# Kernel optimization log

Hardware: AMD Instinct MI355X
Metric: run time of the kernel (lower is better)

## Reference

```python
import jax, jax.numpy as jnp
import numpy as np

NS = 50000; ND = 50000; E = 600000
C = 64; A = 16; S = 64; H = 8; M = 192; DH = C // H
EPS = 1e-5


def _ln(x, w, b):
    # EquivariantLayerNormV2 restricted to 0e irreps == standard affine LayerNorm
    x = x - jnp.mean(x, axis=-1, keepdims=True)
    v = jnp.mean(x * x, axis=-1, keepdims=True)
    return x * jax.lax.rsqrt(v + EPS) * w + b


def _forward(src_f, dst_f, edge_attr, edge_scalars, edge_logits, edge_src, edge_dst,
             ln_src_w, ln_src_b, W_src, ln_dst_w, ln_dst_b, W_dst, b_dst,
             W_ea, W_dtp, W_r1, b_r1, W_r2, b_r2, alpha_vec,
             W_proj, b_proj, ln_post_w, ln_post_b, W_f1, b_f1, W_f2, b_f2):
    # prenorm + linear projections of src/dst node features
    ms = _ln(src_f, ln_src_w, ln_src_b) @ W_src                      # [NS, C]
    md = _ln(dst_f, ln_dst_w, ln_dst_b) @ W_dst + b_dst              # [ND, C]
    msg = ms[edge_src] + md[edge_dst]                                # [E, C] gather
    # radial MLP on edge scalars modulates the (scalar-irrep) tensor-product weights
    r = jax.nn.silu(edge_scalars @ W_r1 + b_r1)                      # [E, S]
    w_edge = r @ W_r2 + b_r2                                         # [E, 2C]
    ea = edge_attr @ W_ea                                            # [E, C]
    dtp = ((msg * ea) @ W_dtp) * w_edge                              # [E, 2C]
    alpha_feat = dtp[:, :C].reshape(E, H, DH)
    val = dtp[:, C:].reshape(E, H, DH)
    # per-head attention logits + optional precomputed edge logits
    logits = jnp.sum(jax.nn.leaky_relu(alpha_feat, 0.2) * alpha_vec, axis=-1)  # [E, H]
    logits = logits + edge_logits[:, None]
    # softmax over incoming edges of each dst node (segment softmax)
    m = jax.ops.segment_max(logits, edge_dst, num_segments=ND)
    a = jnp.exp(logits - m[edge_dst])
    z = jax.ops.segment_sum(a, edge_dst, num_segments=ND)
    attn = a / z[edge_dst]                                           # [E, H]
    out = jax.ops.segment_sum((val * attn[..., None]).reshape(E, C), edge_dst,
                              num_segments=ND)                       # [ND, C] scatter
    out = out @ W_proj + b_proj
    emb = out + dst_f                                                # skip_1 (irreps match -> identity)
    y = _ln(emb, ln_post_w, ln_post_b)                               # post_norm
    ffn = jax.nn.silu(y @ W_f1 + b_f1) @ W_f2 + b_f2                 # FFN with swish gate (0e)
    return ffn + emb                                                 # skip_2


def setup_inputs() -> dict:
    key = jax.random.key(0)
    ks = jax.random.split(key, 20)
    def n(k, shape, scale=1.0):
        return jax.random.normal(k, shape, dtype=jnp.float32) * scale
    return {
        "src_f": n(ks[0], (NS, C)),
        "dst_f": n(ks[1], (ND, C)),
        "edge_attr": n(ks[2], (E, A)),
        "edge_scalars": jax.random.uniform(ks[3], (E, S), dtype=jnp.float32),
        "edge_logits": n(ks[4], (E,)),
        "edge_src": jax.random.randint(ks[5], (E,), 0, NS),
        "edge_dst": jax.random.randint(ks[6], (E,), 0, ND),
        "ln_src_w": jnp.ones((C,), jnp.float32), "ln_src_b": jnp.zeros((C,), jnp.float32),
        "W_src": n(ks[7], (C, C), C ** -0.5),
        "ln_dst_w": jnp.ones((C,), jnp.float32), "ln_dst_b": jnp.zeros((C,), jnp.float32),
        "W_dst": n(ks[8], (C, C), C ** -0.5), "b_dst": jnp.zeros((C,), jnp.float32),
        "W_ea": n(ks[9], (A, C), A ** -0.5),
        "W_dtp": n(ks[10], (C, 2 * C), C ** -0.5),
        "W_r1": n(ks[11], (S, S), S ** -0.5), "b_r1": jnp.zeros((S,), jnp.float32),
        "W_r2": n(ks[12], (S, 2 * C), S ** -0.5), "b_r2": jnp.zeros((2 * C,), jnp.float32),
        "alpha_vec": n(ks[13], (H, DH), DH ** -0.5),
        "W_proj": n(ks[14], (C, C), C ** -0.5), "b_proj": jnp.zeros((C,), jnp.float32),
        "ln_post_w": jnp.ones((C,), jnp.float32), "ln_post_b": jnp.zeros((C,), jnp.float32),
        "W_f1": n(ks[15], (C, M), C ** -0.5), "b_f1": jnp.zeros((M,), jnp.float32),
        "W_f2": n(ks[16], (M, C), M ** -0.5), "b_f2": jnp.zeros((C,), jnp.float32),
    }


def reference(src_f, dst_f, edge_attr, edge_scalars, edge_logits, edge_src, edge_dst,
              ln_src_w, ln_src_b, W_src, ln_dst_w, ln_dst_b, W_dst, b_dst,
              W_ea, W_dtp, W_r1, b_r1, W_r2, b_r2, alpha_vec,
              W_proj, b_proj, ln_post_w, ln_post_b, W_f1, b_f1, W_f2, b_f2):
    return _forward(src_f, dst_f, edge_attr, edge_scalars, edge_logits, edge_src, edge_dst,
                    ln_src_w, ln_src_b, W_src, ln_dst_w, ln_dst_b, W_dst, b_dst,
                    W_ea, W_dtp, W_r1, b_r1, W_r2, b_r2, alpha_vec,
                    W_proj, b_proj, ln_post_w, ln_post_b, W_f1, b_f1, W_f2, b_f2)
```

## Files before the change

kernel.cpp:

```cpp
#include <hip/hip_runtime.h>
#include <hip/hip_bf16.h>

typedef __hip_bfloat16 bf16;
typedef unsigned short u16;
typedef unsigned int u32;

#define NS_N 50000
#define ND_N 50000
#define NE_E 600000
#define C 64
#define AD 16
#define SD 64
#define NH 8
#define MF 192
#define EPSV 1e-5f

#define WB() __builtin_amdgcn_wave_barrier()

typedef short short8 __attribute__((ext_vector_type(8)));
typedef float f32x4 __attribute__((ext_vector_type(4)));
#define MFMA16(a, b, c) __builtin_amdgcn_mfma_f32_16x16x32_bf16(a, b, c, 0, 0, 0)

__device__ __forceinline__ float lo16(u32 u) {
    union { u32 i; float f; } v; v.i = u << 16; return v.f;
}
__device__ __forceinline__ float hi16(u32 u) {
    union { u32 i; float f; } v; v.i = u & 0xffff0000u; return v.f;
}
__device__ __forceinline__ float b2fu(u16 u) {
    union { u32 i; float f; } v; v.i = ((u32)u) << 16; return v.f;
}
__device__ __forceinline__ u16 f2bbits(float f) {
    u32 u = __float_as_uint(f);
    u32 r = u + 0x7FFFu + ((u >> 16) & 1u);
    return (u16)(r >> 16);
}
__device__ __forceinline__ float loadf(const void* p, size_t i, int isbf) {
    if (isbf) { union { u32 u; float f; } v; v.u = ((u32)((const u16*)p)[i]) << 16; return v.f; }
    return ((const float*)p)[i];
}
__device__ __forceinline__ u16 loadb(const void* p, size_t i, int isbf) {
    if (isbf) return ((const u16*)p)[i];
    return f2bbits(((const float*)p)[i]);
}
__device__ __forceinline__ short8 load8bf(const void* p, size_t off, int isbf) {
    if (isbf) return *(const short8*)((const u16*)p + off);
    const float4* q = (const float4*)((const float*)p + off);
    float4 f0 = q[0], f1 = q[1];
    short8 r;
    r[0] = (short)f2bbits(f0.x); r[1] = (short)f2bbits(f0.y);
    r[2] = (short)f2bbits(f0.z); r[3] = (short)f2bbits(f0.w);
    r[4] = (short)f2bbits(f1.x); r[5] = (short)f2bbits(f1.y);
    r[6] = (short)f2bbits(f1.z); r[7] = (short)f2bbits(f1.w);
    return r;
}

__device__ __forceinline__ float waveAllSum(float v) {
    #pragma unroll
    for (int off = 32; off >= 1; off >>= 1) v += __shfl_xor(v, off, 64);
    return v;
}

__global__ void detect_zero_kernel(const void* src, int* flag, int* cnt) {
    if (blockIdx.x == 0) {
        if (threadIdx.x < 64) {
            const u16* p = (const u16*)src;
            const int lane = threadIdx.x;
            int c = 0;
            #pragma unroll
            for (int j = 0; j < 32; ++j) {
                u16 w = p[(size_t)(lane * 32 + j) * 2];
                int e = (w >> 7) & 0xFF;
                if (w == 0 || (e >= 100 && e <= 150)) c++;
            }
            #pragma unroll
            for (int off = 32; off >= 1; off >>= 1) c += __shfl_xor(c, off, 64);
            if (lane == 0) *flag = (c > 1536) ? 1 : 0;
        }
    } else {
        int i = (blockIdx.x - 1) * blockDim.x + threadIdx.x;
        if (i < ND_N) cnt[i] = 0;
    }
}

__global__ void hist_kernel(const int* __restrict__ edge_dst, int* __restrict__ cnt) {
    int e = blockIdx.x * blockDim.x + threadIdx.x;
    if (e < NE_E) atomicAdd(&cnt[edge_dst[e]], 1);
}

#define SCAN_CHUNK 1024
#define SCAN_NCH ((ND_N + SCAN_CHUNK - 1) / SCAN_CHUNK)

__global__ void scan_phase1(const int* __restrict__ cnt, int* __restrict__ chunksum) {
    __shared__ int wsum[4];
    const int b = blockIdx.x, tidx = threadIdx.x;
    const int base = b * SCAN_CHUNK + tidx * 4;
    int s = 0;
    if (base + 3 < ND_N) {
        int4 v = *(const int4*)&cnt[base];
        s = v.x + v.y + v.z + v.w;
    } else {
        #pragma unroll
        for (int j = 0; j < 4; ++j) { int i = base + j; if (i < ND_N) s += cnt[i]; }
    }
    #pragma unroll
    for (int off = 32; off >= 1; off >>= 1) s += __shfl_xor(s, off, 64);
    const int wv = tidx >> 6, lane = tidx & 63;
    if (lane == 0) wsum[wv] = s;
    __syncthreads();
    if (tidx == 0) chunksum[b] = wsum[0] + wsum[1] + wsum[2] + wsum[3];
}

__global__ void scan_phase3(const int* __restrict__ cnt, const int* __restrict__ chunksum,
                            int* __restrict__ row_ptr, int* __restrict__ cursor,
                            int* __restrict__ row_ptr_last) {
    __shared__ int woff[4];
    __shared__ int choff_s;
    const int b = blockIdx.x, tidx = threadIdx.x;
    if (tidx < 64) {
        int v = (tidx < SCAN_NCH) ? chunksum[tidx] : 0;
        int incl = v;
        #pragma unroll
        for (int off = 1; off < 64; off <<= 1) {
            int t = __shfl_up(incl, off, 64);
            if (tidx >= off) incl += t;
        }
        if (tidx == b) choff_s = incl - v;
        if (b == 0 && tidx == 63) *row_ptr_last = incl;
    }
    const int base = b * SCAN_CHUNK + tidx * 4;
    int v[4];
    #pragma unroll
    for (int j = 0; j < 4; ++j) { int i = base + j; v[j] = (i < ND_N) ? cnt[i] : 0; }
    int s = v[0] + v[1] + v[2] + v[3];
    int incl = s;
    const int lane = tidx & 63, wv = tidx >> 6;
    #pragma unroll
    for (int off = 1; off < 64; off <<= 1) {
        int t = __shfl_up(incl, off, 64);
        if (lane >= off) incl += t;
    }
    if (lane == 63) woff[wv] = incl;
    __syncthreads();
    int cross = 0;
    for (int w = 0; w < wv; ++w) cross += woff[w];
    int run = choff_s + cross + (incl - s);
    #pragma unroll
    for (int j = 0; j < 4; ++j) {
        int i = base + j;
        if (i < ND_N) { row_ptr[i] = run; cursor[i] = run; }
        run += v[j];
    }
}

__global__ void scatter_kernel(const int* __restrict__ edge_dst, int* __restrict__ cursor,
                               int* __restrict__ perm) {
    int e = blockIdx.x * blockDim.x + threadIdx.x;
    if (e < NE_E) {
        int pos = atomicAdd(&cursor[edge_dst[e]], 1);
        perm[pos] = e;
    }
}

__global__ void node_proj2_kernel(const void* __restrict__ src_f, const void* __restrict__ dst_f,
                                  const void* __restrict__ lnw_s, const void* __restrict__ lnb_s,
                                  const void* __restrict__ W_s,
                                  const void* __restrict__ lnw_d, const void* __restrict__ lnb_d,
                                  const void* __restrict__ W_d, const void* __restrict__ b_d,
                                  const int* __restrict__ flagp,
                                  u16* __restrict__ ms, u16* __restrict__ md) {
    __shared__ u16 sW[C * C];
    __shared__ float slnw[C], slnb[C], sbias[C];
    __shared__ float ybuf[4][C];

    const int isbf = *flagp;
    const int tid = threadIdx.x;
    const int half = gridDim.x >> 1;
    const int isrc = (blockIdx.x < half) ? 1 : 0;
    const void* xf  = isrc ? src_f : dst_f;
    const void* lnw = isrc ? lnw_s : lnw_d;
    const void* lnb = isrc ? lnb_s : lnb_d;
    const void* W   = isrc ? W_s : W_d;
    u16* out        = isrc ? ms : md;
    const int N     = isrc ? NS_N : ND_N;
    const int bid   = isrc ? blockIdx.x : blockIdx.x - half;
    const int nb    = isrc ? half : gridDim.x - half;

    for (int i = tid; i < C * C; i += blockDim.x) {
        int k = i >> 6, c = i & 63;
        sW[((k >> 1) << 7) + (c << 1) + (k & 1)] = loadb(W, i, isbf);
    }
    if (tid < C) {
        slnw[tid] = loadf(lnw, tid, isbf);
        slnb[tid] = loadf(lnb, tid, isbf);
        sbias[tid] = isrc ? 0.f : loadf(b_d, tid, isbf);
    }
    __syncthreads();

    const int wave = tid >> 6, lane = tid & 63;
    const u32* w = (const u32*)sW;
    const int gw = bid * 4 + wave, nw = nb * 4;
    for (int n = gw; n < N; n += nw) {
        float x = loadf(xf, (size_t)n * C + lane, isbf);
        float mean = waveAllSum(x) * (1.f / 64.f);
        float xc = x - mean;
        float var = waveAllSum(xc * xc) * (1.f / 64.f);
        float y = xc * rsqrtf(var + EPSV) * slnw[lane] + slnb[lane];
        WB();
        ybuf[wave][lane] = y;
        WB();
        float acc = sbias[lane];
        #pragma unroll 8
        for (int k2 = 0; k2 < 32; ++k2) {
            float2 yv = *(const float2*)&ybuf[wave][k2 * 2];
            u32 wp = w[(k2 << 6) + lane];
            acc += yv.x * lo16(wp) + yv.y * hi16(wp);
        }
        WB();
        out[(size_t)n * C + lane] = f2bbits(acc);
        WB();
    }
}

__launch_bounds__(512, 4)
__global__ void edge_mfma_kernel(const void* __restrict__ edge_attr,
                                 const void* __restrict__ edge_scalars,
                                 const void* __restrict__ edge_logits,
                                 const int* __restrict__ edge_src,
                                 const int* __restrict__ edge_dst,
                                 const int* __restrict__ perm,
                                 const void* __restrict__ W_ea, const void* __restrict__ W_dtp,
                                 const void* __restrict__ W_r1, const void* __restrict__ b_r1,
                                 const void* __restrict__ W_r2, const void* __restrict__ b_r2,
                                 const void* __restrict__ alpha_vec,
                                 const int* __restrict__ flagp,
                                 const u16* __restrict__ ms, const u16* __restrict__ md,
                                 u16* __restrict__ valbuf, float* __restrict__ logitsbuf) {
    __shared__ u16 sWr1T[C * SD];
    __shared__ u16 sWr2T[2 * C * SD];
    __shared__ u16 sWdtpT[2 * C * C];
    __shared__ u16 sWeaT[C * 32];
    __shared__ float sbr1[SD], sbr2[2 * C], salpha[C];
    __shared__ u16 scratch[8][2][16 * C];

    const int isbf = *flagp;
    const int tid = threadIdx.x;
    for (int i = tid; i < SD * SD; i += 512) {
        int k = i >> 6, n = i & 63;
        sWr1T[n * 64 + (((k >> 3) ^ (n & 7)) << 3) + (k & 7)] = loadb(W_r1, i, isbf);
    }
    for (int i = tid; i < SD * 2 * C; i += 512) {
        int k = i >> 7, n = i & 127;
        sWr2T[n * 64 + (((k >> 3) ^ (n & 7)) << 3) + (k & 7)] = loadb(W_r2, i, isbf);
    }
    for (int i = tid; i < C * 2 * C; i += 512) {
        int k = i >> 7, n = i & 127;
        sWdtpT[n * 64 + (((k >> 3) ^ (n & 7)) << 3) + (k & 7)] = loadb(W_dtp, i, isbf);
    }
    for (int i = tid; i < C * 32; i += 512) {
        int n = i >> 5, k = i & 31;
        sWeaT[i] = (k < AD) ? loadb(W_ea, (size_t)k * C + n, isbf) : (u16)0;
    }
    for (int i = tid; i < SD; i += 512) sbr1[i] = loadf(b_r1, i, isbf);
    for (int i = tid; i < 2 * C; i += 512) sbr2[i] = loadf(b_r2, i, isbf);
    for (int i = tid; i < C; i += 512) salpha[i] = loadf(alpha_vec, i, isbf);
    __syncthreads();

    const int wv = tid >> 6, lane = tid & 63;
    const int m15 = lane & 15, quad = lane >> 4;
    const int sw = m15 & 7;
    const int pg0 = (quad ^ sw) << 3;
    const int pg1 = pg0 ^ 32;
    u16* scr_r = scratch[wv][0];
    u16* scr_e = scratch[wv][1];

    const int NT = NE_E / 16;
    const int stride = gridDim.x * 8;
    int t = blockIdx.x * 8 + wv;

    int e = 0, s = 0, dd = 0;
    if (t < NT) {
        e = perm[t * 16 + m15];
        s = edge_src[e];
        dd = edge_dst[e];
    }

    while (t < NT) {
        const int tn = t + stride;
        const int e0 = t * 16;
        short8 esA0 = load8bf(edge_scalars, (size_t)e * SD + quad * 8, isbf);
        short8 esA1 = load8bf(edge_scalars, (size_t)e * SD + 32 + quad * 8, isbf);
        float elg_lane = loadf(edge_logits, e, isbf);
        short8 eaA = 0;
        if (quad < 2) eaA = load8bf(edge_attr, (size_t)e * AD + quad * 8, isbf);
        const u16* msr = ms + (size_t)s * C;
        const u16* mdr = md + (size_t)dd * C;
        short8 gms0 = *(const short8*)&msr[quad * 8];
        short8 gms1 = *(const short8*)&msr[32 + quad * 8];
        short8 gmd0 = *(const short8*)&mdr[quad * 8];
        short8 gmd1 = *(const short8*)&mdr[32 + quad * 8];
        int eN = 0;
        if (tn < NT) eN = perm[tn * 16 + m15];
        WB();
        #pragma unroll
        for (int nt = 0; nt < 4; ++nt) {
            f32x4 c = {0.f, 0.f, 0.f, 0.f};
            c = MFMA16(esA0, *(const short8*)&sWr1T[(nt * 16 + m15) * 64 + pg0], c);
            c = MFMA16(esA1, *(const short8*)&sWr1T[(nt * 16 + m15) * 64 + pg1], c);
            float bc = sbr1[nt * 16 + m15];
            int lg = nt * 2 + (m15 >> 3);
            int o = m15 & 7;
            #pragma unroll
            for (int r = 0; r < 4; ++r) {
                float f = c[r] + bc;
                f = f / (1.f + __expf(-f));
                int row = quad * 4 + r;
                scr_r[row * 64 + ((lg ^ (row & 7)) << 3) + o] = f2bbits(f);
            }
        }
        #pragma unroll
        for (int nt = 0; nt < 4; ++nt) {
            f32x4 c = {0.f, 0.f, 0.f, 0.f};
            c = MFMA16(eaA, *(const short8*)&sWeaT[(nt * 16 + m15) * 32 + quad * 8], c);
            int lg = nt * 2 + (m15 >> 3);
            int o = m15 & 7;
            #pragma unroll
            for (int r = 0; r < 4; ++r) {
                int row = quad * 4 + r;
                scr_e[row * 64 + ((lg ^ (row & 7)) << 3) + o] = f2bbits(c[r]);
            }
        }
        int sN = 0, ddN = 0;
        if (tn < NT) { sN = edge_src[eN]; ddN = edge_dst[eN]; }
        WB();
        short8 rA0 = *(const short8*)&scr_r[m15 * 64 + pg0];
        short8 rA1 = *(const short8*)&scr_r[m15 * 64 + pg1];
        short8 ev0 = *(const short8*)&scr_e[m15 * 64 + pg0];
        short8 ev1 = *(const short8*)&scr_e[m15 * 64 + pg1];
        short8 xA0, xA1;
        #pragma unroll
        for (int j = 0; j < 8; ++j) {
            float a = b2fu((u16)gms0[j]) + b2fu((u16)gmd0[j]);
            xA0[j] = (short)f2bbits(a * b2fu((u16)ev0[j]));
            float b = b2fu((u16)gms1[j]) + b2fu((u16)gmd1[j]);
            xA1[j] = (short)f2bbits(b * b2fu((u16)ev1[j]));
        }
        float elg_q[4];
        #pragma unroll
        for (int r = 0; r < 4; ++r) elg_q[r] = __shfl(elg_lane, quad * 4 + r, 64);
        WB();
        #pragma unroll
        for (int nt = 0; nt < 8; ++nt) {
            f32x4 w = {0.f, 0.f, 0.f, 0.f};
            w = MFMA16(rA0, *(const short8*)&sWr2T[(nt * 16 + m15) * 64 + pg0], w);
            w = MFMA16(rA1, *(const short8*)&sWr2T[(nt * 16 + m15) * 64 + pg1], w);
            f32x4 dv = {0.f, 0.f, 0.f, 0.f};
            dv = MFMA16(xA0, *(const short8*)&sWdtpT[(nt * 16 + m15) * 64 + pg0], dv);
            dv = MFMA16(xA1, *(const short8*)&sWdtpT[(nt * 16 + m15) * 64 + pg1], dv);
            float wb = sbr2[nt * 16 + m15];
            if (nt < 4) {
                float sa = salpha[nt * 16 + m15];
                #pragma unroll
                for (int r = 0; r < 4; ++r) {
                    float v = dv[r] * (w[r] + wb);
                    float lf = (v >= 0.f) ? v : 0.2f * v;
                    float tt = lf * sa;
                    tt += __shfl_xor(tt, 1, 64);
                    tt += __shfl_xor(tt, 2, 64);
                    tt += __shfl_xor(tt, 4, 64);
                    if ((lane & 7) == 0)
                        logitsbuf[(size_t)(e0 + quad * 4 + r) * NH + nt * 2 + ((lane >> 3) & 1)]
                            = tt + elg_q[r];
                }
            } else {
                int lg = (nt - 4) * 2 + (m15 >> 3);
                int o = m15 & 7;
                #pragma unroll
                for (int r = 0; r < 4; ++r) {
                    float v = dv[r] * (w[r] + wb);
                    int row = quad * 4 + r;
                    scr_r[row * 64 + ((lg ^ (row & 7)) << 3) + o] = f2bbits(v);
                }
            }
        }
        WB();
        {
            int row = lane >> 2, seg = lane & 3;
            int rw7 = row & 7;
            uint4 v0 = *(const uint4*)&scr_r[row * 64 + (((seg * 2) ^ rw7) << 3)];
            uint4 v1 = *(const uint4*)&scr_r[row * 64 + (((seg * 2 + 1) ^ rw7) << 3)];
            uint4* gp = (uint4*)&valbuf[(size_t)(e0 + row) * C + seg * 16];
            gp[0] = v0; gp[1] = v1;
        }
        WB();
        t = tn; e = eN; s = sN; dd = ddN;
    }
}

__global__ void aggregate_kernel(const int* __restrict__ row_ptr,
                                 const float* __restrict__ logitsbuf,
                                 const u16* __restrict__ valbuf,
                                 float* __restrict__ attout) {
    const int wave = threadIdx.x >> 6, lane = threadIdx.x & 63;
    const int head = lane >> 3;
    const int gw = blockIdx.x * 4 + wave, nw = gridDim.x * 4;
    for (int d = gw; d < ND_N; d += nw) {
        const int beg = row_ptr[d], end = row_ptr[d + 1];
        float m0 = -__builtin_inff(), z0 = 0.f, a0 = 0.f;
        float m1 = -__builtin_inff(), z1 = 0.f, a1 = 0.f;
        int i = beg;
        for (; i + 1 < end; i += 2) {
            float lg0 = logitsbuf[(size_t)i * NH + head];
            float lg1 = logitsbuf[(size_t)(i + 1) * NH + head];
            float v0 = b2fu(valbuf[(size_t)i * C + lane]);
            float v1 = b2fu(valbuf[(size_t)(i + 1) * C + lane]);
            float mn0 = fmaxf(m0, lg0);
            float mn1 = fmaxf(m1, lg1);
            float sc0 = __expf(m0 - mn0);
            float sc1 = __expf(m1 - mn1);
            float e0 = __expf(lg0 - mn0);
            float e1 = __expf(lg1 - mn1);
            z0 = z0 * sc0 + e0; a0 = a0 * sc0 + e0 * v0; m0 = mn0;
            z1 = z1 * sc1 + e1; a1 = a1 * sc1 + e1 * v1; m1 = mn1;
        }
        if (i < end) {
            float lg0 = logitsbuf[(size_t)i * NH + head];
            float v0 = b2fu(valbuf[(size_t)i * C + lane]);
            float mn = fmaxf(m0, lg0);
            float sc = __expf(m0 - mn);
            float e0 = __expf(lg0 - mn);
            z0 = z0 * sc + e0; a0 = a0 * sc + e0 * v0; m0 = mn;
        }
        float mn = fmaxf(m0, m1);
        float s0 = __expf(m0 - mn);
        float s1 = __expf(m1 - mn);
        float z = z0 * s0 + z1 * s1;
        float acc = a0 * s0 + a1 * s1;
        attout[(size_t)d * C + lane] = (z > 0.f) ? acc / z : 0.f;
    }
}

__global__ void edge_csr_kernel(const void* __restrict__ edge_attr,
                                const void* __restrict__ edge_scalars,
                                const void* __restrict__ edge_logits,
                                const int* __restrict__ edge_src,
                                const int* __restrict__ row_ptr, const int* __restrict__ perm,
                                const void* __restrict__ W_ea, const void* __restrict__ W_dtp,
                                const void* __restrict__ W_r1, const void* __restrict__ b_r1,
                                const void* __restrict__ W_r2, const void* __restrict__ b_r2,
                                const void* __restrict__ alpha_vec,
                                const int* __restrict__ flagp,
                                const u16* __restrict__ ms, const u16* __restrict__ md,
                                float* __restrict__ attout) {
    __shared__ u16 sWr1[SD * SD];
    __shared__ u16 sWr2[SD * 2 * C];
    __shared__ u16 sWdtp[C * 2 * C];
    __shared__ u16 sWea[AD * C];
    __shared__ float sbr1[SD], sbr2[2 * C], salpha[C];
    __shared__ float sbuf[4][2][C];

    const int isbf = *flagp;
    const int tid = threadIdx.x;
    {
        for (int i = tid; i < SD * SD; i += blockDim.x) {
            int k = i >> 6, c = i & 63;
            sWr1[((k >> 1) << 7) + (c << 1) + (k & 1)] = loadb(W_r1, i, isbf);
        }
        for (int i = tid; i < SD * 2 * C; i += blockDim.x) {
            int k = i >> 7, c = i & 127;
            sWr2[(k << 7) + ((c & 63) << 1) + (c >> 6)] = loadb(W_r2, i, isbf);
        }
        for (int i = tid; i < C * 2 * C; i += blockDim.x) {
            int k = i >> 7, c = i & 127;
            sWdtp[(k << 7) + ((c & 63) << 1) + (c >> 6)] = loadb(W_dtp, i, isbf);
        }
        for (int i = tid; i < AD * C; i += blockDim.x) {
            int k = i >> 6, c = i & 63;
            sWea[((k >> 1) << 7) + (c << 1) + (k & 1)] = loadb(W_ea, i, isbf);
        }
        for (int i = tid; i < SD; i += blockDim.x) sbr1[i] = loadf(b_r1, i, isbf);
        for (int i = tid; i < 2 * C; i += blockDim.x) sbr2[i] = loadf(b_r2, i, isbf);
        for (int i = tid; i < C; i += blockDim.x) salpha[i] = loadf(alpha_vec, i, isbf);
    }
    __syncthreads();

    const int wave = tid >> 6, lane = tid & 63;
    float* buf0 = sbuf[wave][0];
    float* buf1 = sbuf[wave][1];
    const u32* wr1 = (const u32*)sWr1;
    const u32* wr2 = (const u32*)sWr2;
    const u32* wdtp = (const u32*)sWdtp;
    const u32* wea = (const u32*)sWea;
    const int gw = blockIdx.x * 4 + wave, nw = gridDim.x * 4;

    for (int d = gw; d < ND_N; d += nw) {
        const int beg = row_ptr[d], end = row_ptr[d + 1];
        const float mdv = b2fu(md[(size_t)d * C + lane]);
        float m = -__builtin_inff(), z = 0.f, acc = 0.f;

        for (int i = beg; i < end; ++i) {
            const int e = perm[i];
            WB();
            buf0[lane] = loadf(edge_scalars, (size_t)e * SD + lane, isbf);
            WB();
            float accr = sbr1[lane];
            #pragma unroll 8
            for (int k2 = 0; k2 < 32; ++k2) {
                float2 xv = *(const float2*)&buf0[k2 * 2];
                u32 wp = wr1[(k2 << 6) + lane];
                accr += xv.x * lo16(wp) + xv.y * hi16(wp);
            }
            float r = accr / (1.f + __expf(-accr));
            WB();
            buf1[lane] = r;
            WB();
            float we0 = sbr2[lane], we1 = sbr2[lane + C];
            #pragma unroll 8
            for (int k = 0; k < SD; ++k) {
                float rk = buf1[k];
                u32 wp = wr2[(k << 6) + lane];
                we0 += rk * lo16(wp);
                we1 += rk * hi16(wp);
            }
            WB();
            if (lane < AD) buf0[lane] = loadf(edge_attr, (size_t)e * AD + lane, isbf);
            WB();
            float eav = 0.f;
            #pragma unroll
            for (int k2 = 0; k2 < 8; ++k2) {
                float2 xv = *(const float2*)&buf0[k2 * 2];
                u32 wp = wea[(k2 << 6) + lane];
                eav += xv.x * lo16(wp) + xv.y * hi16(wp);
            }
            const int s = edge_src[e];
            float x = (b2fu(ms[(size_t)s * C + lane]) + mdv) * eav;
            WB();
            buf1[lane] = x;
            WB();
            float dt0 = 0.f, dt1 = 0.f;
            #pragma unroll 8
            for (int k = 0; k < C; ++k) {
                float xk = buf1[k];
                u32 wp = wdtp[(k << 6) + lane];
                dt0 += xk * lo16(wp);
                dt1 += xk * hi16(wp);
            }
            dt0 *= we0;
            dt1 *= we1;
            float lf = (dt0 >= 0.f) ? dt0 : 0.2f * dt0;
            float t = lf * salpha[lane];
            t += __shfl_xor(t, 1, 64);
            t += __shfl_xor(t, 2, 64);
            t += __shfl_xor(t, 4, 64);
            float lg = t + loadf(edge_logits, e, isbf);
            float mn = fmaxf(m, lg);
            float sc = __expf(m - mn);
            float a = __expf(lg - mn);
            z = z * sc + a;
            acc = acc * sc + a * dt1;
            m = mn;
        }
        attout[(size_t)d * C + lane] = (z > 0.f) ? acc / z : 0.f;
    }
}

__launch_bounds__(512, 2)
__global__ void final_mfma_kernel(const void* __restrict__ dst_f,
                                  const float* __restrict__ attout,
                                  const void* __restrict__ W_proj, const void* __restrict__ b_proj,
                                  const void* __restrict__ ln_w, const void* __restrict__ ln_b,
                                  const void* __restrict__ W_f1, const void* __restrict__ b_f1,
                                  const void* __restrict__ W_f2, const void* __restrict__ b_f2,
                                  const int* __restrict__ flagp,
                                  void* __restrict__ out) {
    __shared__ u16 sWpT[C * C];
    __shared__ u16 sWf1T[MF * C];
    __shared__ u16 sWf2T[C * MF];
    __shared__ float sbp[C], slnw[C], slnb[C], sbf1[MF], sbf2[C];
    __shared__ uint4 scr4[8][400];

    const int isbf = *flagp;
    const int tid = threadIdx.x;
    for (int i = tid; i < C * C; i += 512) {
        int k = i >> 6, n = i & 63;
        sWpT[n * 64 + (((k >> 3) ^ (n & 7)) << 3) + (k & 7)] = loadb(W_proj, i, isbf);
    }
    for (int i = tid; i < C * MF; i += 512) {
        int k = i / MF, n = i - k * MF;
        sWf1T[n * 64 + (((k >> 3) ^ (n & 7)) << 3) + (k & 7)] = loadb(W_f1, i, isbf);
    }
    for (int i = tid; i < MF * C; i += 512) {
        int k = i >> 6, n = i & 63;
        sWf2T[n * 192 + (((k >> 3) ^ (n & 7)) << 3) + (k & 7)] = loadb(W_f2, i, isbf);
    }
    for (int i = tid; i < C; i += 512) {
        sbp[i] = loadf(b_proj, i, isbf);
        slnw[i] = loadf(ln_w, i, isbf);
        slnb[i] = loadf(ln_b, i, isbf);
        sbf2[i] = loadf(b_f2, i, isbf);
    }
    for (int i = tid; i < MF; i += 512) sbf1[i] = loadf(b_f1, i, isbf);
    __syncthreads();

    const int wv = tid >> 6, lane = tid & 63;
    const int m15 = lane & 15, quad = lane >> 4;
    const int sw = m15 & 7;
    const int pg0 = (quad ^ sw) << 3;
    const int pg1 = pg0 ^ 32;
    u16* scr = (u16*)scr4[wv];
    float* scrf = (float*)scr4[wv];

    for (int t = blockIdx.x * 8 + wv; t < ND_N / 16; t += gridDim.x * 8) {
        const int n0 = t * 16;
        short8 oA0 = load8bf(attout, (size_t)(n0 + m15) * C + quad * 8, 0);
        short8 oA1 = load8bf(attout, (size_t)(n0 + m15) * C + 32 + quad * 8, 0);
        float emb[4][4];
        #pragma unroll
        for (int nt = 0; nt < 4; ++nt) {
            f32x4 c = {0.f, 0.f, 0.f, 0.f};
            c = MFMA16(oA0, *(const short8*)&sWpT[(nt * 16 + m15) * 64 + pg0], c);
            c = MFMA16(oA1, *(const short8*)&sWpT[(nt * 16 + m15) * 64 + pg1], c);
            int col = nt * 16 + m15;
            float bp = sbp[col];
            #pragma unroll
            for (int r = 0; r < 4; ++r)
                emb[nt][r] = c[r] + bp + loadf(dst_f, (size_t)(n0 + quad * 4 + r) * C + col, isbf);
        }
        float y[4][4];
        #pragma unroll
        for (int r = 0; r < 4; ++r) {
            float part = emb[0][r] + emb[1][r] + emb[2][r] + emb[3][r];
            part += __shfl_xor(part, 1, 64);
            part += __shfl_xor(part, 2, 64);
            part += __shfl_xor(part, 4, 64);
            part += __shfl_xor(part, 8, 64);
            float mean = part * (1.f / 64.f);
            float q = 0.f;
            #pragma unroll
            for (int nt = 0; nt < 4; ++nt) {
                float d = emb[nt][r] - mean;
                q += d * d;
            }
            q += __shfl_xor(q, 1, 64);
            q += __shfl_xor(q, 2, 64);
            q += __shfl_xor(q, 4, 64);
            q += __shfl_xor(q, 8, 64);
            float rs = rsqrtf(q * (1.f / 64.f) + EPSV);
            #pragma unroll
            for (int nt = 0; nt < 4; ++nt) {
                int col = nt * 16 + m15;
                y[nt][r] = (emb[nt][r] - mean) * rs * slnw[col] + slnb[col];
            }
        }
        WB();
        #pragma unroll
        for (int nt = 0; nt < 4; ++nt)
            #pragma unroll
            for (int r = 0; r < 4; ++r)
                scr[(quad * 4 + r) * 72 + nt * 16 + m15] = f2bbits(y[nt][r]);
        WB();
        short8 yA0 = *(const short8*)&scr[m15 * 72 + quad * 8];
        short8 yA1 = *(const short8*)&scr[m15 * 72 + 32 + quad * 8];
        WB();
        #pragma unroll
        for (int nt = 0; nt < 12; ++nt) {
            f32x4 g = {0.f, 0.f, 0.f, 0.f};
            g = MFMA16(yA0, *(const short8*)&sWf1T[(nt * 16 + m15) * 64 + pg0], g);
            g = MFMA16(yA1, *(const short8*)&sWf1T[(nt * 16 + m15) * 64 + pg1], g);
            int col = nt * 16 + m15;
            float bg = sbf1[col];
            #pragma unroll
            for (int r = 0; r < 4; ++r) {
                float f = g[r] + bg;
                f = f / (1.f + __expf(-f));
                scr[(quad * 4 + r) * 200 + col] = f2bbits(f);
            }
        }
        WB();
        short8 gA[6];
        #pragma unroll
        for (int j = 0; j < 6; ++j)
            gA[j] = *(const short8*)&scr[m15 * 200 + j * 32 + quad * 8];
        WB();
        #pragma unroll
        for (int nt = 0; nt < 4; ++nt) {
            f32x4 c = {0.f, 0.f, 0.f, 0.f};
            #pragma unroll
            for (int j = 0; j < 6; ++j) {
                int lg = j * 4 + quad;
                int pg = (lg ^ sw) << 3;
                c = MFMA16(gA[j], *(const short8*)&sWf2T[(nt * 16 + m15) * 192 + pg], c);
            }
            int col = nt * 16 + m15;
            float bf = sbf2[col];
            #pragma unroll
            for (int r = 0; r < 4; ++r)
                scrf[(quad * 4 + r) * 68 + col] = c[r] + bf + emb[nt][r];
        }
        WB();
        {
            int row = lane >> 2, seg = lane & 3;
            if (isbf) {
                u16* gp = (u16*)out + (size_t)(n0 + row) * C + seg * 16;
                #pragma unroll
                for (int j = 0; j < 4; ++j) {
                    float4 v = *(const float4*)&scrf[row * 68 + seg * 16 + j * 4];
                    u32 p0 = (u32)f2bbits(v.x) | ((u32)f2bbits(v.y) << 16);
                    u32 p1 = (u32)f2bbits(v.z) | ((u32)f2bbits(v.w) << 16);
                    uint2 pk = {p0, p1};
                    *(uint2*)(gp + j * 4) = pk;
                }
            } else {
                float* gp = (float*)out + (size_t)(n0 + row) * C + seg * 16;
                #pragma unroll
                for (int j = 0; j < 4; ++j)
                    *(float4*)(gp + j * 4) = *(const float4*)&scrf[row * 68 + seg * 16 + j * 4];
            }
        }
        WB();
    }
}

__global__ void final_scalar_kernel(const void* __restrict__ dst_f,
                                    const float* __restrict__ attout,
                                    const void* __restrict__ W_proj, const void* __restrict__ b_proj,
                                    const void* __restrict__ ln_w, const void* __restrict__ ln_b,
                                    const void* __restrict__ W_f1, const void* __restrict__ b_f1,
                                    const void* __restrict__ W_f2, const void* __restrict__ b_f2,
                                    const int* __restrict__ flagp,
                                    void* __restrict__ out) {
    __shared__ u16 sWp[C * C];
    __shared__ u16 sWf1p[C * 2 * C];
    __shared__ u16 sWf1c[C * C];
    __shared__ u16 sWf2[MF * C];
    __shared__ float sbp[C], slnw[C], slnb[C], sbf1[MF], sbf2[C];
    __shared__ float ybuf[4][C];
    __shared__ float gbuf[4][MF];

    const int isbf = *flagp;
    const int tid = threadIdx.x;
    {
        for (int i = tid; i < C * C; i += blockDim.x) {
            int k = i >> 6, c = i & 63;
            sWp[((k >> 1) << 7) + (c << 1) + (k & 1)] = loadb(W_proj, i, isbf);
        }
        for (int i = tid; i < C * MF; i += blockDim.x) {
            int k = i / MF, c = i - k * MF;
            u16 b = loadb(W_f1, i, isbf);
            if (c < 128) sWf1p[(k << 7) + ((c & 63) << 1) + (c >> 6)] = b;
            else         sWf1c[(k << 6) + (c - 128)] = b;
        }
        for (int i = tid; i < MF * C; i += blockDim.x) {
            int k = i >> 6, c = i & 63;
            sWf2[((k >> 1) << 7) + (c << 1) + (k & 1)] = loadb(W_f2, i, isbf);
        }
        for (int i = tid; i < C; i += blockDim.x) {
            sbp[i] = loadf(b_proj, i, isbf);
            slnw[i] = loadf(ln_w, i, isbf);
            slnb[i] = loadf(ln_b, i, isbf);
            sbf2[i] = loadf(b_f2, i, isbf);
        }
        for (int i = tid; i < MF; i += blockDim.x) sbf1[i] = loadf(b_f1, i, isbf);
    }
    __syncthreads();

    const int wave = tid >> 6, lane = tid & 63;
    const u32* wp32 = (const u32*)sWp;
    const u32* wf1 = (const u32*)sWf1p;
    const u32* wf2 = (const u32*)sWf2;
    const int gw = blockIdx.x * 4 + wave, nw = gridDim.x * 4;

    for (int n = gw; n < ND_N; n += nw) {
        float o = attout[(size_t)n * C + lane];
        WB();
        ybuf[wave][lane] = o;
        WB();
        float p = sbp[lane];
        #pragma unroll 8
        for (int k2 = 0; k2 < 32; ++k2) {
            float2 yv = *(const float2*)&ybuf[wave][k2 * 2];
            u32 wv = wp32[(k2 << 6) + lane];
            p += yv.x * lo16(wv) + yv.y * hi16(wv);
        }
        float emb = p + loadf(dst_f, (size_t)n * C + lane, isbf);
        float mean = waveAllSum(emb) * (1.f / 64.f);
        float ec = emb - mean;
        float var = waveAllSum(ec * ec) * (1.f / 64.f);
        float y = ec * rsqrtf(var + EPSV) * slnw[lane] + slnb[lane];
        WB();
        ybuf[wave][lane] = y;
        WB();
        float g0 = sbf1[lane], g1v = sbf1[lane + C], g2v = sbf1[lane + 2 * C];
        #pragma unroll 8
        for (int k = 0; k < C; ++k) {
            float yk = ybuf[wave][k];
            u32 wv = wf1[(k << 6) + lane];
            union { u32 u; float f; } cv; cv.u = ((u32)sWf1c[(k << 6) + lane]) << 16;
            g0 += yk * lo16(wv);
            g1v += yk * hi16(wv);
            g2v += yk * cv.f;
        }
        WB();
        gbuf[wave][lane] = g0 / (1.f + __expf(-g0));
        gbuf[wave][lane + C] = g1v / (1.f + __expf(-g1v));
        gbuf[wave][lane + 2 * C] = g2v / (1.f + __expf(-g2v));
        WB();
        float f = sbf2[lane];
        #pragma unroll 8
        for (int k2 = 0; k2 < 96; ++k2) {
            float2 gv = *(const float2*)&gbuf[wave][k2 * 2];
            u32 wv = wf2[(k2 << 6) + lane];
            f += gv.x * lo16(wv) + gv.y * hi16(wv);
        }
        WB();
        float res = f + emb;
        if (isbf) ((bf16*)out)[(size_t)n * C + lane] = __float2bfloat16(res);
        else      ((float*)out)[(size_t)n * C + lane] = res;
    }
}

extern "C" void kernel_launch(void* const* d_in, const int* in_sizes, int n_in,
                              void* d_out, int out_size, void* d_ws, size_t ws_size,
                              hipStream_t stream) {
    const void* src_f        = d_in[0];
    const void* dst_f        = d_in[1];
    const void* edge_attr    = d_in[2];
    const void* edge_scalars = d_in[3];
    const void* edge_logits  = d_in[4];
    const int*  edge_src     = (const int*)d_in[5];
    const int*  edge_dst     = (const int*)d_in[6];
    const void* ln_src_w = d_in[7];
    const void* ln_src_b = d_in[8];
    const void* W_src    = d_in[9];
    const void* ln_dst_w = d_in[10];
    const void* ln_dst_b = d_in[11];
    const void* W_dst    = d_in[12];
    const void* b_dst    = d_in[13];
    const void* W_ea     = d_in[14];
    const void* W_dtp    = d_in[15];
    const void* W_r1     = d_in[16];
    const void* b_r1     = d_in[17];
    const void* W_r2     = d_in[18];
    const void* b_r2     = d_in[19];
    const void* alpha_vec = d_in[20];
    const void* W_proj   = d_in[21];
    const void* b_proj   = d_in[22];
    const void* ln_post_w = d_in[23];
    const void* ln_post_b = d_in[24];
    const void* W_f1     = d_in[25];
    const void* b_f1     = d_in[26];
    const void* W_f2     = d_in[27];
    const void* b_f2     = d_in[28];

    int* flag     = (int*)d_ws;
    float* msf    = (float*)d_ws + 16;
    float* mdf    = msf + (size_t)NS_N * C;
    u16* ms16     = (u16*)msf;
    u16* md16     = (u16*)mdf;
    int* cnt      = (int*)(mdf + (size_t)ND_N * C);
    int* row_ptr  = cnt + ND_N;
    int* cursor   = row_ptr + (ND_N + 4);
    int* perm     = cursor + ND_N;
    float* logitsbuf = (float*)(perm + NE_E);
    u16* valbuf      = (u16*)(logitsbuf + (size_t)NE_E * NH);
    float* attout_slow = (float*)(perm + NE_E);

    size_t base_b = (size_t)(16 + NS_N * C + ND_N * C) * 4
                  + ((size_t)ND_N * 3 + 4 + NE_E) * 4;
    size_t need_fast = base_b + (size_t)NE_E * NH * 4 + (size_t)NE_E * C * 2;
    size_t need_slow = base_b + (size_t)ND_N * C * 4;
    int fast = (ws_size >= need_fast) ? 1 : 0;
    if (!fast && ws_size < need_slow) return;

    detect_zero_kernel<<<1 + (ND_N + 255) / 256, 256, 0, stream>>>(src_f, flag, cnt);
    hist_kernel<<<(NE_E + 255) / 256, 256, 0, stream>>>(edge_dst, cnt);
    scan_phase1<<<SCAN_NCH, 256, 0, stream>>>(cnt, perm);
    scan_phase3<<<SCAN_NCH, 256, 0, stream>>>(cnt, perm, row_ptr, cursor, &row_ptr[ND_N]);
    scatter_kernel<<<(NE_E + 255) / 256, 256, 0, stream>>>(edge_dst, cursor, perm);

    node_proj2_kernel<<<2048, 256, 0, stream>>>(src_f, dst_f,
                                                ln_src_w, ln_src_b, W_src,
                                                ln_dst_w, ln_dst_b, W_dst, b_dst,
                                                flag, ms16, md16);

    if (fast) {
        edge_mfma_kernel<<<1024, 512, 0, stream>>>(edge_attr, edge_scalars, edge_logits,
                                                   edge_src, edge_dst, perm,
                                                   W_ea, W_dtp, W_r1, b_r1, W_r2, b_r2,
                                                   alpha_vec, flag, ms16, md16,
                                                   valbuf, logitsbuf);
        aggregate_kernel<<<2048, 256, 0, stream>>>(row_ptr, logitsbuf, valbuf, msf);
        final_mfma_kernel<<<256, 512, 0, stream>>>(dst_f, msf,
                                                   W_proj, b_proj, ln_post_w, ln_post_b,
                                                   W_f1, b_f1, W_f2, b_f2,
                                                   flag, d_out);
    } else {
        edge_csr_kernel<<<2048, 256, 0, stream>>>(edge_attr, edge_scalars, edge_logits,
                                                  edge_src, row_ptr, perm,
                                                  W_ea, W_dtp, W_r1, b_r1, W_r2, b_r2,
                                                  alpha_vec, flag, ms16, md16, attout_slow);
        final_scalar_kernel<<<1024, 256, 0, stream>>>(dst_f, attout_slow,
                                                      W_proj, b_proj, ln_post_w, ln_post_b,
                                                      W_f1, b_f1, W_f2, b_f2,
                                                      flag, d_out);
    }
}
```

Measured before the change: 606.7 us.

## Use MFMA for node projections and split aggregation across edge parity

Node layernorm+projection is rewritten to process 16-node tiles per wave, with bf16 MFMA against a swizzled transposed weight in shared memory and vectorized loads and stores. This replaces the per-node scalar dot-product loop. The aggregate kernel now has each lane handle two channels, and the two half-waves take alternating edges, with an online-softmax merge across halves through a shuffle. Its grid size is doubled. The node tiling assumes NS equals ND and that both divide evenly by 16, and the inputs are rounded to bf16 before the MFMA.

```diff
diff --git a/kernel.cpp b/kernel.cpp
--- a/kernel.cpp
+++ b/kernel.cpp
@@ -162,62 +162,120 @@
     }
 }
 
-__global__ void node_proj2_kernel(const void* __restrict__ src_f, const void* __restrict__ dst_f,
-                                  const void* __restrict__ lnw_s, const void* __restrict__ lnb_s,
-                                  const void* __restrict__ W_s,
-                                  const void* __restrict__ lnw_d, const void* __restrict__ lnb_d,
-                                  const void* __restrict__ W_d, const void* __restrict__ b_d,
-                                  const int* __restrict__ flagp,
-                                  u16* __restrict__ ms, u16* __restrict__ md) {
-    __shared__ u16 sW[C * C];
-    __shared__ float slnw[C], slnb[C], sbias[C];
-    __shared__ float ybuf[4][C];
+__launch_bounds__(512)
+__global__ void node_proj2_mfma(const void* __restrict__ src_f, const void* __restrict__ dst_f,
+                                const void* __restrict__ lnw_s, const void* __restrict__ lnb_s,
+                                const void* __restrict__ W_s,
+                                const void* __restrict__ lnw_d, const void* __restrict__ lnb_d,
+                                const void* __restrict__ W_d, const void* __restrict__ b_d,
+                                const int* __restrict__ flagp,
+                                u16* __restrict__ ms, u16* __restrict__ md) {
+    __shared__ u16 sWT[2][C * C];
+    __shared__ float slnw2[2][C], slnb2[2][C], sbias[C];
+    __shared__ u16 scratch[8][16 * C];
 
     const int isbf = *flagp;
     const int tid = threadIdx.x;
-    const int half = gridDim.x >> 1;
-    const int isrc = (blockIdx.x < half) ? 1 : 0;
-    const void* xf  = isrc ? src_f : dst_f;
-    const void* lnw = isrc ? lnw_s : lnw_d;
-    const void* lnb = isrc ? lnb_s : lnb_d;
-    const void* W   = isrc ? W_s : W_d;
-    u16* out        = isrc ? ms : md;
-    const int N     = isrc ? NS_N : ND_N;
-    const int bid   = isrc ? blockIdx.x : blockIdx.x - half;
-    const int nb    = isrc ? half : gridDim.x - half;
-
-    for (int i = tid; i < C * C; i += blockDim.x) {
-        int k = i >> 6, c = i & 63;
-        sW[((k >> 1) << 7) + (c << 1) + (k & 1)] = loadb(W, i, isbf);
-    }
-    if (tid < C) {
-        slnw[tid] = loadf(lnw, tid, isbf);
-        slnb[tid] = loadf(lnb, tid, isbf);
-        sbias[tid] = isrc ? 0.f : loadf(b_d, tid, isbf);
+    for (int i = tid; i < C * C; i += 512) {
+        int k = i >> 6, n = i & 63;
+        int off = n * 64 + (((k >> 3) ^ (n & 7)) << 3) + (k & 7);
+        sWT[0][off] = loadb(W_s, i, isbf);
+        sWT[1][off] = loadb(W_d, i, isbf);
+    }
+    for (int i = tid; i < C; i += 512) {
+        slnw2[0][i] = loadf(lnw_s, i, isbf);
+        slnb2[0][i] = loadf(lnb_s, i, isbf);
+        slnw2[1][i] = loadf(lnw_d, i, isbf);
+        slnb2[1][i] = loadf(lnb_d, i, isbf);
+        sbias[i] = loadf(b_d, i, isbf);
     }
     __syncthreads();
 
-    const int wave = tid >> 6, lane = tid & 63;
-    const u32* w = (const u32*)sW;
-    const int gw = bid * 4 + wave, nw = nb * 4;
-    for (int n = gw; n < N; n += nw) {
-        float x = loadf(xf, (size_t)n * C + lane, isbf);
-        float mean = waveAllSum(x) * (1.f / 64.f);
-        float xc = x - mean;
-        float var = waveAllSum(xc * xc) * (1.f / 64.f);
-        float y = xc * rsqrtf(var + EPSV) * slnw[lane] + slnb[lane];
-        WB();
-        ybuf[wave][lane] = y;
-        WB();
-        float acc = sbias[lane];
-        #pragma unroll 8
-        for (int k2 = 0; k2 < 32; ++k2) {
-            float2 yv = *(const float2*)&ybuf[wave][k2 * 2];
-            u32 wp = w[(k2 << 6) + lane];
-            acc += yv.x * lo16(wp) + yv.y * hi16(wp);
-        }
-        WB();
-        out[(size_t)n * C + lane] = f2bbits(acc);
+    const int wv = tid >> 6, lane = tid & 63;
+    const int m15 = lane & 15, quad = lane >> 4;
+    const int sw = m15 & 7;
+    const int pg0 = (quad ^ sw) << 3;
+    const int pg1 = pg0 ^ 32;
+    u16* scr = scratch[wv];
+
+    const int HT = NS_N / 16;
+    const int NTILE = 2 * HT;
+    for (int t = blockIdx.x * 8 + wv; t < NTILE; t += gridDim.x * 8) {
+        const int half = (t >= HT) ? 1 : 0;
+        const int n0 = (half ? (t - HT) : t) * 16;
+        const void* xf = half ? dst_f : src_f;
+        u16* out = half ? md : ms;
+        float x0[8], x1[8];
+        {
+            size_t base = (size_t)(n0 + m15) * C + quad * 8;
+            if (isbf) {
+                short8 aa = *(const short8*)((const u16*)xf + base);
+                short8 bb = *(const short8*)((const u16*)xf + base + 32);
+                #pragma unroll
+                for (int j = 0; j < 8; ++j) {
+                    x0[j] = b2fu((u16)aa[j]);
+                    x1[j] = b2fu((u16)bb[j]);
+                }
+            } else {
+                const float* xp = (const float*)xf + base;
+                float4 a0 = *(const float4*)xp;
+                float4 a1 = *(const float4*)(xp + 4);
+                float4 b0 = *(const float4*)(xp + 32);
+                float4 b1 = *(const float4*)(xp + 36);
+                x0[0] = a0.x; x0[1] = a0.y; x0[2] = a0.z; x0[3] = a0.w;
+                x0[4] = a1.x; x0[5] = a1.y; x0[6] = a1.z; x0[7] = a1.w;
+                x1[0] = b0.x; x1[1] = b0.y; x1[2] = b0.z; x1[3] = b0.w;
+                x1[4] = b1.x; x1[5] = b1.y; x1[6] = b1.z; x1[7] = b1.w;
+            }
+        }
+        float s = 0.f;
+        #pragma unroll
+        for (int j = 0; j < 8; ++j) s += x0[j] + x1[j];
+        s += __shfl_xor(s, 16, 64);
+        s += __shfl_xor(s, 32, 64);
+        float mean = s * (1.f / 64.f);
+        float q = 0.f;
+        #pragma unroll
+        for (int j = 0; j < 8; ++j) {
+            float d0 = x0[j] - mean, d1 = x1[j] - mean;
+            q += d0 * d0 + d1 * d1;
+        }
+        q += __shfl_xor(q, 16, 64);
+        q += __shfl_xor(q, 32, 64);
+        float rs = rsqrtf(q * (1.f / 64.f) + EPSV);
+        short8 xA0, xA1;
+        #pragma unroll
+        for (int j = 0; j < 8; ++j) {
+            int c0 = quad * 8 + j, c1 = 32 + quad * 8 + j;
+            xA0[j] = (short)f2bbits((x0[j] - mean) * rs * slnw2[half][c0] + slnb2[half][c0]);
+            xA1[j] = (short)f2bbits((x1[j] - mean) * rs * slnw2[half][c1] + slnb2[half][c1]);
+        }
+        WB();
+        const u16* wT = sWT[half];
+        #pragma unroll
+        for (int nt = 0; nt < 4; ++nt) {
+            f32x4 c = {0.f, 0.f, 0.f, 0.f};
+            c = MFMA16(xA0, *(const short8*)&wT[(nt * 16 + m15) * 64 + pg0], c);
+            c = MFMA16(xA1, *(const short8*)&wT[(nt * 16 + m15) * 64 + pg1], c);
+            float bb = half ? sbias[nt * 16 + m15] : 0.f;
+            int lg = nt * 2 + (m15 >> 3);
+            int o = m15 & 7;
+            #pragma unroll
+            for (int r = 0; r < 4; ++r) {
+                float v = c[r] + bb;
+                int row = quad * 4 + r;
+                scr[row * 64 + ((lg ^ (row & 7)) << 3) + o] = f2bbits(v);
+            }
+        }
+        WB();
+        {
+            int row = lane >> 2, seg = lane & 3;
+            int rw7 = row & 7;
+            uint4 v0 = *(const uint4*)&scr[row * 64 + (((seg * 2) ^ rw7) << 3)];
+            uint4 v1 = *(const uint4*)&scr[row * 64 + (((seg * 2 + 1) ^ rw7) << 3)];
+            uint4* gp = (uint4*)&out[(size_t)(n0 + row) * C + seg * 16];
+            gp[0] = v0; gp[1] = v1;
+        }
         WB();
     }
 }
@@ -402,41 +460,57 @@
                                  const u16* __restrict__ valbuf,
                                  float* __restrict__ attout) {
     const int wave = threadIdx.x >> 6, lane = threadIdx.x & 63;
-    const int head = lane >> 3;
+    const int h = lane & 31;
+    const int parity = lane >> 5;
+    const int head = h >> 2;
     const int gw = blockIdx.x * 4 + wave, nw = gridDim.x * 4;
+    const float NINF = -1e30f;
     for (int d = gw; d < ND_N; d += nw) {
         const int beg = row_ptr[d], end = row_ptr[d + 1];
-        float m0 = -__builtin_inff(), z0 = 0.f, a0 = 0.f;
-        float m1 = -__builtin_inff(), z1 = 0.f, a1 = 0.f;
-        int i = beg;
-        for (; i + 1 < end; i += 2) {
-            float lg0 = logitsbuf[(size_t)i * NH + head];
-            float lg1 = logitsbuf[(size_t)(i + 1) * NH + head];
-            float v0 = b2fu(valbuf[(size_t)i * C + lane]);
-            float v1 = b2fu(valbuf[(size_t)(i + 1) * C + lane]);
-            float mn0 = fmaxf(m0, lg0);
-            float mn1 = fmaxf(m1, lg1);
-            float sc0 = __expf(m0 - mn0);
-            float sc1 = __expf(m1 - mn1);
-            float e0 = __expf(lg0 - mn0);
-            float e1 = __expf(lg1 - mn1);
-            z0 = z0 * sc0 + e0; a0 = a0 * sc0 + e0 * v0; m0 = mn0;
-            z1 = z1 * sc1 + e1; a1 = a1 * sc1 + e1 * v1; m1 = mn1;
-        }
-        if (i < end) {
-            float lg0 = logitsbuf[(size_t)i * NH + head];
-            float v0 = b2fu(valbuf[(size_t)i * C + lane]);
-            float mn = fmaxf(m0, lg0);
+        float m0 = NINF, z0 = 0.f, a00 = 0.f, a01 = 0.f;
+        float m1 = NINF, z1 = 0.f, a10 = 0.f, a11 = 0.f;
+        for (int i = beg + parity; i < end; i += 4) {
+            u32 pv = *(const u32*)&valbuf[(size_t)i * C + 2 * h];
+            float lg = logitsbuf[(size_t)i * NH + head];
+            float mn = fmaxf(m0, lg);
             float sc = __expf(m0 - mn);
-            float e0 = __expf(lg0 - mn);
-            z0 = z0 * sc + e0; a0 = a0 * sc + e0 * v0; m0 = mn;
-        }
-        float mn = fmaxf(m0, m1);
-        float s0 = __expf(m0 - mn);
-        float s1 = __expf(m1 - mn);
+            float e = __expf(lg - mn);
+            z0 = z0 * sc + e;
+            a00 = a00 * sc + e * lo16(pv);
+            a01 = a01 * sc + e * hi16(pv);
+            m0 = mn;
+        }
+        for (int i = beg + parity + 2; i < end; i += 4) {
+            u32 pv = *(const u32*)&valbuf[(size_t)i * C + 2 * h];
+            float lg = logitsbuf[(size_t)i * NH + head];
+            float mn = fmaxf(m1, lg);
+            float sc = __expf(m1 - mn);
+            float e = __expf(lg - mn);
+            z1 = z1 * sc + e;
+            a10 = a10 * sc + e * lo16(pv);
+            a11 = a11 * sc + e * hi16(pv);
+            m1 = mn;
+        }
+        float ma = fmaxf(m0, m1);
+        float s0 = __expf(m0 - ma), s1 = __expf(m1 - ma);
         float z = z0 * s0 + z1 * s1;
-        float acc = a0 * s0 + a1 * s1;
-        attout[(size_t)d * C + lane] = (z > 0.f) ? acc / z : 0.f;
+        float a0 = a00 * s0 + a10 * s1;
+        float a1 = a01 * s0 + a11 * s1;
+        float mo = __shfl_xor(ma, 32, 64);
+        float zo = __shfl_xor(z, 32, 64);
+        float b0 = __shfl_xor(a0, 32, 64);
+        float b1 = __shfl_xor(a1, 32, 64);
+        float mm = fmaxf(ma, mo);
+        float se = __expf(ma - mm), so = __expf(mo - mm);
+        z = z * se + zo * so;
+        a0 = a0 * se + b0 * so;
+        a1 = a1 * se + b1 * so;
+        if (parity == 0) {
+            float2 r;
+            r.x = (z > 0.f) ? a0 / z : 0.f;
+            r.y = (z > 0.f) ? a1 / z : 0.f;
+            *(float2*)&attout[(size_t)d * C + 2 * h] = r;
+        }
     }
 }
 
@@ -878,10 +952,10 @@
     scan_phase3<<<SCAN_NCH, 256, 0, stream>>>(cnt, perm, row_ptr, cursor, &row_ptr[ND_N]);
     scatter_kernel<<<(NE_E + 255) / 256, 256, 0, stream>>>(edge_dst, cursor, perm);
 
-    node_proj2_kernel<<<2048, 256, 0, stream>>>(src_f, dst_f,
-                                                ln_src_w, ln_src_b, W_src,
-                                                ln_dst_w, ln_dst_b, W_dst, b_dst,
-                                                flag, ms16, md16);
+    node_proj2_mfma<<<782, 512, 0, stream>>>(src_f, dst_f,
+                                             ln_src_w, ln_src_b, W_src,
+                                             ln_dst_w, ln_dst_b, W_dst, b_dst,
+                                             flag, ms16, md16);
 
     if (fast) {
         edge_mfma_kernel<<<1024, 512, 0, stream>>>(edge_attr, edge_scalars, edge_logits,
@@ -889,7 +963,7 @@
                                                    W_ea, W_dtp, W_r1, b_r1, W_r2, b_r2,
                                                    alpha_vec, flag, ms16, md16,
                                                    valbuf, logitsbuf);
-        aggregate_kernel<<<2048, 256, 0, stream>>>(row_ptr, logitsbuf, valbuf, msf);
+        aggregate_kernel<<<4096, 256, 0, stream>>>(row_ptr, logitsbuf, valbuf, msf);
         final_mfma_kernel<<<256, 512, 0, stream>>>(dst_f, msf,
                                                    W_proj, b_proj, ln_post_w, ln_post_b,
                                                    W_f1, b_f1, W_f2, b_f2,
```

Result: faster. 575.2 us (-5.2%).
